# Kernel optimization log

Measured on AMD Instinct MI355X. Metric: run time of the kernel, lower is better.

## Reference

```python
import jax, jax.numpy as jnp
import numpy as np

D_MODEL = 1024
H = 16
D_K = D_MODEL // H


def setup_inputs() -> dict:
    key = jax.random.key(0)
    ks = jax.random.split(key, 12)
    B, S = 2, 2048
    scale = 1.0 / np.sqrt(D_MODEL)
    inp = {
        "q": jax.random.normal(ks[0], (B, S, D_MODEL), jnp.float32),
        "k": jax.random.normal(ks[1], (B, S, D_MODEL), jnp.float32),
        "v": jax.random.normal(ks[2], (B, S, D_MODEL), jnp.float32),
        "mask": jnp.ones((B, 1, S, S), jnp.int32),
        "w_q": jax.random.normal(ks[3], (D_MODEL, D_MODEL), jnp.float32) * scale,
        "b_q": jnp.zeros((D_MODEL,), jnp.float32),
        "w_k": jax.random.normal(ks[4], (D_MODEL, D_MODEL), jnp.float32) * scale,
        "b_k": jnp.zeros((D_MODEL,), jnp.float32),
        "w_v": jax.random.normal(ks[5], (D_MODEL, D_MODEL), jnp.float32) * scale,
        "b_v": jnp.zeros((D_MODEL,), jnp.float32),
        "w_o": jax.random.normal(ks[6], (D_MODEL, D_MODEL), jnp.float32) * scale,
        "b_o": jnp.zeros((D_MODEL,), jnp.float32),
    }
    return inp


def _split_heads(x):
    B, S, _ = x.shape
    return x.reshape(B, S, H, D_K).transpose(0, 2, 1, 3)  # [B,H,S,Dk]


def reference(q, k, v, mask, w_q, b_q, w_k, b_k, w_v, b_v, w_o, b_o):
    # Linear projections (torch Linear: x @ W^T + b)
    query = _split_heads(q @ w_q.T + b_q)
    key = _split_heads(k @ w_k.T + b_k)
    value = _split_heads(v @ w_v.T + b_v)

    # scaled dot-product attention: [B,H,S,S]
    scores = jnp.einsum("bhqd,bhkd->bhqk", query, key) / jnp.sqrt(
        jnp.asarray(D_K, query.dtype)
    )
    scores = jnp.where(mask == 0, jnp.asarray(-1e9, scores.dtype), scores)
    attn = jax.nn.softmax(scores, axis=-1)  # dropout p=0.0 -> identity
    out = jnp.einsum("bhqk,bhkd->bhqd", attn, value)  # [B,H,S,Dk]

    # combine heads -> [B,S,D_MODEL]
    B = out.shape[0]
    out = out.transpose(0, 2, 1, 3).reshape(B, -1, D_MODEL)
    return out @ w_o.T + b_o
```

## Files before the change

### kernel.cpp

```cpp
#include <hip/hip_runtime.h>
#include <hip/hip_bf16.h>

#define S_LEN 2048
#define BATCH 2
#define NH    16
#define DK    64
#define DM    1024

typedef __bf16 bf16x8 __attribute__((ext_vector_type(8)));
typedef float  f32x4  __attribute__((ext_vector_type(4)));
typedef ushort u16x8  __attribute__((ext_vector_type(8)));

__device__ __forceinline__ float bf2f(ushort u) {
    union { unsigned int i; float f; } v; v.i = ((unsigned int)u) << 16; return v.f;
}
__device__ __forceinline__ ushort f2bf(float f) {
    union { float f; unsigned int i; } v; v.f = f;
    unsigned int u = v.i;
    unsigned int r = u + 0x7fff + ((u >> 16) & 1);
    return (ushort)(r >> 16);
}
__device__ __forceinline__ ushort f2bf_fast(float f) {
    union { float f; unsigned int i; } v; v.f = f;
    return (ushort)((v.i + 0x8000u) >> 16);
}

__global__ void detect(const ushort* __restrict__ q, int* __restrict__ flags) {
    __shared__ int red[256];
    int tid = threadIdx.x;
    int cnt = 0;
    for (int i = tid; i < 2048; i += 256) {
        ushort e = q[2 * i];
        int ex = (e >> 7) & 0xFF;
        if (ex == 0 || (ex >= 107 && ex <= 147)) cnt++;
    }
    red[tid] = cnt;
    __syncthreads();
    for (int s = 128; s > 0; s >>= 1) {
        if (tid < s) red[tid] += red[tid + s];
        __syncthreads();
    }
    if (tid == 0) {
        flags[0] = (red[0] < 1229) ? 1 : 0;
        flags[1] = 0;
    }
}

__global__ void mask_check(const int* __restrict__ mask, int* __restrict__ flags) {
    const int total = BATCH * S_LEN * S_LEN / 4;
    int idx = blockIdx.x * blockDim.x + threadIdx.x;
    int stride = gridDim.x * blockDim.x;
    bool bad = false;
    for (int i = idx; i < total; i += stride) {
        int4 v = ((const int4*)mask)[i];
        if (v.x == 0 || v.y == 0 || v.z == 0 || v.w == 0) bad = true;
    }
    if (__any(bad)) {
        if ((threadIdx.x & 63) == 0) atomicOr(&flags[1], 1);
    }
}

#define NJOBS 11
struct CvtJobs { const void* src[NJOBS]; };

__device__ __constant__ const int g_cum[NJOBS + 1] = {
    0, 4194304, 8388608, 12582912, 13631488, 14680064, 15728640,
    16777216, 16778240, 16779264, 16780288, 16781312
};

__global__ __launch_bounds__(256) void convert_all(CvtJobs J, ushort* __restrict__ conv,
                                                   const int* __restrict__ flags) {
    bool isf32 = flags[0] != 0;
    const int total_chunks = 16781312 / 8;
    int c = blockIdx.x * blockDim.x + threadIdx.x;
    int stride = gridDim.x * blockDim.x;
    for (; c < total_chunks; c += stride) {
        int e = c * 8;
        int j = 0;
        while (j + 1 < NJOBS + 1 && e >= g_cum[j + 1]) j++;
        int local = e - g_cum[j];
        if (isf32) {
            const float* s = (const float*)J.src[j] + local;
            f32x4 a = *(const f32x4*)s;
            f32x4 b = *(const f32x4*)(s + 4);
            ushort o[8] = { f2bf(a[0]), f2bf(a[1]), f2bf(a[2]), f2bf(a[3]),
                            f2bf(b[0]), f2bf(b[1]), f2bf(b[2]), f2bf(b[3]) };
            *(ushort4*)&conv[e]     = *(ushort4*)&o[0];
            *(ushort4*)&conv[e + 4] = *(ushort4*)&o[4];
        } else {
            const ushort* s = (const ushort*)J.src[j] + local;
            bf16x8 v = *(const bf16x8*)s;
            *(bf16x8*)&conv[e] = v;
        }
    }
}

struct GArg { const ushort* x; const ushort* w; const ushort* bias; void* y; int split; };

#define ASTR 40

__global__ __launch_bounds__(256) void gemm_bt(GArg a0, GArg a1, GArg a2,
                                               const int* __restrict__ flags) {
    GArg A = (blockIdx.z == 0) ? a0 : (blockIdx.z == 1 ? a1 : a2);
    const int K = 1024, N = 1024;
    __shared__ ushort As[128 * ASTR];
    __shared__ ushort Bs[128 * ASTR];

    int tid = threadIdx.x;
    int w = tid >> 6, lane = tid & 63;
    int wm = (w >> 1) * 64, wn = (w & 1) * 64;
    int m0 = blockIdx.y * 128, n0 = blockIdx.x * 128;

    f32x4 acc[4][4] = {};

    int row0 = tid >> 2;
    int pos  = (tid & 3) * 8;
    int row1 = row0 + 64;

    int fr = lane & 15;
    int qd = lane >> 4;

    const ushort* xp = A.x;
    const ushort* wp = A.w;

    for (int k0 = 0; k0 < K; k0 += 32) {
        bf16x8 ax0 = *(const bf16x8*)&xp[(size_t)(m0 + row0) * K + k0 + pos];
        bf16x8 ax1 = *(const bf16x8*)&xp[(size_t)(m0 + row1) * K + k0 + pos];
        bf16x8 bx0 = *(const bf16x8*)&wp[(size_t)(n0 + row0) * K + k0 + pos];
        bf16x8 bx1 = *(const bf16x8*)&wp[(size_t)(n0 + row1) * K + k0 + pos];
        __syncthreads();
        *(bf16x8*)&As[row0 * ASTR + pos] = ax0;
        *(bf16x8*)&As[row1 * ASTR + pos] = ax1;
        *(bf16x8*)&Bs[row0 * ASTR + pos] = bx0;
        *(bf16x8*)&Bs[row1 * ASTR + pos] = bx1;
        __syncthreads();

        bf16x8 af[4], bfr[4];
#pragma unroll
        for (int i = 0; i < 4; i++) {
            af[i]  = *(const bf16x8*)&As[(wm + i * 16 + fr) * ASTR + qd * 8];
            bfr[i] = *(const bf16x8*)&Bs[(wn + i * 16 + fr) * ASTR + qd * 8];
        }
#pragma unroll
        for (int i = 0; i < 4; i++)
#pragma unroll
            for (int j = 0; j < 4; j++)
                acc[i][j] = __builtin_amdgcn_mfma_f32_16x16x32_bf16(af[i], bfr[j], acc[i][j], 0, 0, 0);
    }

    bool isf32 = flags[0] != 0;
    int crow = qd * 4;
    int ccol = fr;
#pragma unroll
    for (int j = 0; j < 4; j++) {
        int n_g = n0 + wn + j * 16 + ccol;
        float bias = bf2f(A.bias[n_g]);
#pragma unroll
        for (int i = 0; i < 4; i++) {
#pragma unroll
            for (int r = 0; r < 4; r++) {
                int m_g = m0 + wm + i * 16 + crow + r;
                float val = acc[i][j][r] + bias;
                if (A.split) {
                    int bb = m_g >> 11, s = m_g & 2047;
                    int h = n_g >> 6, d = n_g & 63;
                    ((ushort*)A.y)[((size_t)(bb * NH + h) * S_LEN + s) * DK + d] = f2bf(val);
                } else if (isf32) {
                    ((float*)A.y)[(size_t)m_g * N + n_g] = val;
                } else {
                    ((ushort*)A.y)[(size_t)m_g * N + n_g] = f2bf(val);
                }
            }
        }
    }
}

#define KSTR 80
#define VSTR 72
#define PSTR 76

__global__ __launch_bounds__(256) void attn(const ushort* __restrict__ qp,
                                            const ushort* __restrict__ kp,
                                            const ushort* __restrict__ vp,
                                            const int* __restrict__ mask,
                                            const int* __restrict__ flags,
                                            ushort* __restrict__ ctx) {
    __shared__ ushort Ks[64 * KSTR];
    __shared__ ushort Vt[64 * VSTR];
    __shared__ ushort Pb[4][16 * PSTR];

    int tid = threadIdx.x, w = tid >> 6, lane = tid & 63;
    int bh = blockIdx.y;
    int b = bh >> 4, h = bh & 15;
    int q0 = blockIdx.x * 64;

    const ushort* qb = qp + (size_t)bh * S_LEN * DK;
    const ushort* kb = kp + (size_t)bh * S_LEN * DK;
    const ushort* vb = vp + (size_t)bh * S_LEN * DK;
    const int* mb = mask + (size_t)b * S_LEN * S_LEN;
    bool do_mask = flags[1] != 0;

    int fr = lane & 15;
    int qd = lane >> 4;

    bf16x8 qf[2];
#pragma unroll
    for (int kc = 0; kc < 2; kc++)
        qf[kc] = *(const bf16x8*)&qb[(size_t)(q0 + w * 16 + fr) * DK + kc * 32 + qd * 8];

    f32x4 oacc[4] = {};
    float lrow[4] = {0.f, 0.f, 0.f, 0.f};

    int krow0 = tid >> 3;
    int kpos  = (tid & 7) * 8;
    int krow1 = krow0 + 32;
    int vc0 = w * 8, vc1 = (w + 4) * 8;

    const float cs = 0.125f * 1.44269504f;

    for (int k0 = 0; k0 < S_LEN; k0 += 64) {
        bf16x8 kx0 = *(const bf16x8*)&kb[(size_t)(k0 + krow0) * DK + kpos];
        bf16x8 kx1 = *(const bf16x8*)&kb[(size_t)(k0 + krow1) * DK + kpos];
        u16x8  vx0 = *(const u16x8*)&vb[(size_t)(k0 + lane) * DK + vc0];
        u16x8  vx1 = *(const u16x8*)&vb[(size_t)(k0 + lane) * DK + vc1];
        __syncthreads();
        *(bf16x8*)&Ks[krow0 * KSTR + kpos] = kx0;
        *(bf16x8*)&Ks[krow1 * KSTR + kpos] = kx1;
#pragma unroll
        for (int j = 0; j < 8; j++) {
            Vt[(vc0 + j) * VSTR + lane] = vx0[j];
            Vt[(vc1 + j) * VSTR + lane] = vx1[j];
        }
        __syncthreads();

        f32x4 sc[4] = {};
#pragma unroll
        for (int kc = 0; kc < 2; kc++) {
            bf16x8 kf[4];
#pragma unroll
            for (int ct = 0; ct < 4; ct++)
                kf[ct] = *(const bf16x8*)&Ks[(ct * 16 + fr) * KSTR + kc * 32 + qd * 8];
#pragma unroll
            for (int ct = 0; ct < 4; ct++)
                sc[ct] = __builtin_amdgcn_mfma_f32_16x16x32_bf16(qf[kc], kf[ct], sc[ct], 0, 0, 0);
        }

        if (do_mask) {
#pragma unroll
            for (int ct = 0; ct < 4; ct++)
#pragma unroll
                for (int r = 0; r < 4; r++) {
                    int qr = q0 + w * 16 + qd * 4 + r;
                    int kcid = k0 + ct * 16 + fr;
                    if (mb[(size_t)qr * S_LEN + kcid] == 0) sc[ct][r] = -1e9f;
                }
        }

#pragma unroll
        for (int ct = 0; ct < 4; ct++)
#pragma unroll
            for (int r = 0; r < 4; r++) {
                float p = __builtin_amdgcn_exp2f(fminf(sc[ct][r] * cs, 30.f));
                lrow[r] += p;
                Pb[w][(qd * 4 + r) * PSTR + ct * 16 + fr] = f2bf_fast(p);
            }

#pragma unroll
        for (int kk = 0; kk < 2; kk++) {
            bf16x8 pf = *(const bf16x8*)&Pb[w][fr * PSTR + kk * 32 + qd * 8];
            bf16x8 vf[4];
#pragma unroll
            for (int dt = 0; dt < 4; dt++)
                vf[dt] = *(const bf16x8*)&Vt[(dt * 16 + fr) * VSTR + kk * 32 + qd * 8];
#pragma unroll
            for (int dt = 0; dt < 4; dt++)
                oacc[dt] = __builtin_amdgcn_mfma_f32_16x16x32_bf16(pf, vf[dt], oacc[dt], 0, 0, 0);
        }
    }

#pragma unroll
    for (int r = 0; r < 4; r++) {
        float l = lrow[r];
        l += __shfl_xor(l, 1);
        l += __shfl_xor(l, 2);
        l += __shfl_xor(l, 4);
        l += __shfl_xor(l, 8);
        float inv = 1.0f / l;
        int qr = q0 + w * 16 + qd * 4 + r;
        size_t rowbase = ((size_t)(b * S_LEN + qr) * NH + h) * DK;
#pragma unroll
        for (int dt = 0; dt < 4; dt++)
            ctx[rowbase + dt * 16 + fr] = f2bf(oacc[dt][r] * inv);
    }
}

extern "C" void kernel_launch(void* const* d_in, const int* in_sizes, int n_in,
                              void* d_out, int out_size, void* d_ws, size_t ws_size,
                              hipStream_t stream) {
    const int* mask = (const int*)d_in[3];

    char* ws = (char*)d_ws;
    int*    flags = (int*)ws;
    ushort* conv  = (ushort*)(ws + 4096);
    const size_t conv_bytes = 16781312ull * 2;
    char* p = ws + 4096 + ((conv_bytes + 4095) & ~4095ull);
    size_t sz = (size_t)BATCH * NH * S_LEN * DK * sizeof(ushort);
    ushort* qp  = (ushort*)(p);
    ushort* kp  = (ushort*)(p + sz);
    ushort* vp  = (ushort*)(p + 2 * sz);
    ushort* ctx = (ushort*)(p + 3 * sz);

    ushort* qc  = conv + 0;
    ushort* kc  = conv + 4194304;
    ushort* vc  = conv + 8388608;
    ushort* wqc = conv + 12582912;
    ushort* wkc = conv + 13631488;
    ushort* wvc = conv + 14680064;
    ushort* woc = conv + 15728640;
    ushort* bqc = conv + 16777216;
    ushort* bkc = conv + 16778240;
    ushort* bvc = conv + 16779264;
    ushort* boc = conv + 16780288;

    detect<<<1, 256, 0, stream>>>((const ushort*)d_in[0], flags);
    mask_check<<<1024, 256, 0, stream>>>(mask, flags);

    CvtJobs J;
    J.src[0] = d_in[0];  J.src[1] = d_in[1];  J.src[2] = d_in[2];
    J.src[3] = d_in[4];  J.src[4] = d_in[6];  J.src[5] = d_in[8];
    J.src[6] = d_in[10]; J.src[7] = d_in[5];  J.src[8] = d_in[7];
    J.src[9] = d_in[9];  J.src[10] = d_in[11];
    convert_all<<<2048, 256, 0, stream>>>(J, conv, flags);

    GArg aq{qc, wqc, bqc, qp, 1};
    GArg ak{kc, wkc, bkc, kp, 1};
    GArg av{vc, wvc, bvc, vp, 1};
    gemm_bt<<<dim3(8, 32, 3), 256, 0, stream>>>(aq, ak, av, flags);

    attn<<<dim3(32, 32), 256, 0, stream>>>(qp, kp, vp, mask, flags, ctx);

    GArg ao{ctx, woc, boc, d_out, 0};
    gemm_bt<<<dim3(8, 32, 1), 256, 0, stream>>>(ao, ao, ao, flags);
}
```

Measured before the change: 308.9 us.

## Use async global-to-LDS loads with XOR swizzle, fold softmax scale into Q projection

Replaces the register-staged global-to-shared copies in the projection GEMM and the attention K tile with global_load_lds direct copies, using XOR-swizzled unpadded layouts to avoid bank conflicts. Folds the 1/sqrt(dk)*log2e scale into the Q projection epilogue. In attention, it computes the softmax row sums with an extra MFMA against a ones vector, which removes the shuffle reductions. It also converts P to bf16 by truncation and drops the clamp before exp2. Truncation and the missing clamp could affect accuracy or overflow, and bf16 row sums lose precision.

```diff
diff --git a/kernel.cpp b/kernel.cpp
--- a/kernel.cpp
+++ b/kernel.cpp
@@ -20,9 +20,11 @@
     unsigned int r = u + 0x7fff + ((u >> 16) & 1);
     return (ushort)(r >> 16);
 }
-__device__ __forceinline__ ushort f2bf_fast(float f) {
-    union { float f; unsigned int i; } v; v.f = f;
-    return (ushort)((v.i + 0x8000u) >> 16);
+
+__device__ __forceinline__ void async_copy16(const ushort* g, ushort* l) {
+    __builtin_amdgcn_global_load_lds(
+        (__attribute__((address_space(1))) void*)(g),
+        (__attribute__((address_space(3))) void*)(l), 16, 0, 0);
 }
 
 __global__ void detect(const ushort* __restrict__ q, int* __restrict__ flags) {
@@ -95,16 +97,14 @@
     }
 }
 
-struct GArg { const ushort* x; const ushort* w; const ushort* bias; void* y; int split; };
-
-#define ASTR 40
+struct GArg { const ushort* x; const ushort* w; const ushort* bias; void* y; int split; float scale; };
 
 __global__ __launch_bounds__(256) void gemm_bt(GArg a0, GArg a1, GArg a2,
                                                const int* __restrict__ flags) {
     GArg A = (blockIdx.z == 0) ? a0 : (blockIdx.z == 1 ? a1 : a2);
     const int K = 1024, N = 1024;
-    __shared__ ushort As[128 * ASTR];
-    __shared__ ushort Bs[128 * ASTR];
+    __shared__ ushort As[128 * 32];
+    __shared__ ushort Bs[128 * 32];
 
     int tid = threadIdx.x;
     int w = tid >> 6, lane = tid & 63;
@@ -113,33 +113,30 @@
 
     f32x4 acc[4][4] = {};
 
-    int row0 = tid >> 2;
-    int pos  = (tid & 3) * 8;
-    int row1 = row0 + 64;
+    int srow0 = w * 16 + (lane >> 2);
+    int srow1 = (w + 4) * 16 + (lane >> 2);
+    int schunk = ((lane & 3) ^ ((lane >> 3) & 3)) * 8;
 
     int fr = lane & 15;
     int qd = lane >> 4;
+    int fcp = (qd ^ ((fr >> 1) & 3)) * 8;
 
     const ushort* xp = A.x;
     const ushort* wp = A.w;
 
     for (int k0 = 0; k0 < K; k0 += 32) {
-        bf16x8 ax0 = *(const bf16x8*)&xp[(size_t)(m0 + row0) * K + k0 + pos];
-        bf16x8 ax1 = *(const bf16x8*)&xp[(size_t)(m0 + row1) * K + k0 + pos];
-        bf16x8 bx0 = *(const bf16x8*)&wp[(size_t)(n0 + row0) * K + k0 + pos];
-        bf16x8 bx1 = *(const bf16x8*)&wp[(size_t)(n0 + row1) * K + k0 + pos];
-        __syncthreads();
-        *(bf16x8*)&As[row0 * ASTR + pos] = ax0;
-        *(bf16x8*)&As[row1 * ASTR + pos] = ax1;
-        *(bf16x8*)&Bs[row0 * ASTR + pos] = bx0;
-        *(bf16x8*)&Bs[row1 * ASTR + pos] = bx1;
+        __syncthreads();
+        async_copy16(xp + (size_t)(m0 + srow0) * K + k0 + schunk, &As[w * 512]);
+        async_copy16(xp + (size_t)(m0 + srow1) * K + k0 + schunk, &As[(w + 4) * 512]);
+        async_copy16(wp + (size_t)(n0 + srow0) * K + k0 + schunk, &Bs[w * 512]);
+        async_copy16(wp + (size_t)(n0 + srow1) * K + k0 + schunk, &Bs[(w + 4) * 512]);
         __syncthreads();
 
         bf16x8 af[4], bfr[4];
 #pragma unroll
         for (int i = 0; i < 4; i++) {
-            af[i]  = *(const bf16x8*)&As[(wm + i * 16 + fr) * ASTR + qd * 8];
-            bfr[i] = *(const bf16x8*)&Bs[(wn + i * 16 + fr) * ASTR + qd * 8];
+            af[i]  = *(const bf16x8*)&As[(wm + i * 16 + fr) * 32 + fcp];
+            bfr[i] = *(const bf16x8*)&Bs[(wn + i * 16 + fr) * 32 + fcp];
         }
 #pragma unroll
         for (int i = 0; i < 4; i++)
@@ -160,7 +157,7 @@
 #pragma unroll
             for (int r = 0; r < 4; r++) {
                 int m_g = m0 + wm + i * 16 + crow + r;
-                float val = acc[i][j][r] + bias;
+                float val = (acc[i][j][r] + bias) * A.scale;
                 if (A.split) {
                     int bb = m_g >> 11, s = m_g & 2047;
                     int h = n_g >> 6, d = n_g & 63;
@@ -175,7 +172,6 @@
     }
 }
 
-#define KSTR 80
 #define VSTR 72
 #define PSTR 76
 
@@ -185,7 +181,7 @@
                                             const int* __restrict__ mask,
                                             const int* __restrict__ flags,
                                             ushort* __restrict__ ctx) {
-    __shared__ ushort Ks[64 * KSTR];
+    __shared__ ushort Ks[64 * 64];
     __shared__ ushort Vt[64 * VSTR];
     __shared__ ushort Pb[4][16 * PSTR];
 
@@ -208,24 +204,24 @@
     for (int kc = 0; kc < 2; kc++)
         qf[kc] = *(const bf16x8*)&qb[(size_t)(q0 + w * 16 + fr) * DK + kc * 32 + qd * 8];
 
+    bf16x8 ones;
+#pragma unroll
+    for (int j = 0; j < 8; j++) ones[j] = (__bf16)1.0f;
+
     f32x4 oacc[4] = {};
-    float lrow[4] = {0.f, 0.f, 0.f, 0.f};
-
-    int krow0 = tid >> 3;
-    int kpos  = (tid & 7) * 8;
-    int krow1 = krow0 + 32;
+    f32x4 lacc = {};
+
+    int kschunk = ((lane & 7) ^ ((lane >> 3) & 7)) * 8;
+    int ksrow0 = w * 8 + (lane >> 3);
+    int ksrow1 = (w + 4) * 8 + (lane >> 3);
     int vc0 = w * 8, vc1 = (w + 4) * 8;
 
-    const float cs = 0.125f * 1.44269504f;
-
     for (int k0 = 0; k0 < S_LEN; k0 += 64) {
-        bf16x8 kx0 = *(const bf16x8*)&kb[(size_t)(k0 + krow0) * DK + kpos];
-        bf16x8 kx1 = *(const bf16x8*)&kb[(size_t)(k0 + krow1) * DK + kpos];
-        u16x8  vx0 = *(const u16x8*)&vb[(size_t)(k0 + lane) * DK + vc0];
-        u16x8  vx1 = *(const u16x8*)&vb[(size_t)(k0 + lane) * DK + vc1];
-        __syncthreads();
-        *(bf16x8*)&Ks[krow0 * KSTR + kpos] = kx0;
-        *(bf16x8*)&Ks[krow1 * KSTR + kpos] = kx1;
+        u16x8 vx0 = *(const u16x8*)&vb[(size_t)(k0 + lane) * DK + vc0];
+        u16x8 vx1 = *(const u16x8*)&vb[(size_t)(k0 + lane) * DK + vc1];
+        __syncthreads();
+        async_copy16(&kb[(size_t)(k0 + ksrow0) * DK + kschunk], &Ks[w * 512]);
+        async_copy16(&kb[(size_t)(k0 + ksrow1) * DK + kschunk], &Ks[(w + 4) * 512]);
 #pragma unroll
         for (int j = 0; j < 8; j++) {
             Vt[(vc0 + j) * VSTR + lane] = vx0[j];
@@ -238,8 +234,10 @@
         for (int kc = 0; kc < 2; kc++) {
             bf16x8 kf[4];
 #pragma unroll
-            for (int ct = 0; ct < 4; ct++)
-                kf[ct] = *(const bf16x8*)&Ks[(ct * 16 + fr) * KSTR + kc * 32 + qd * 8];
+            for (int ct = 0; ct < 4; ct++) {
+                int key = ct * 16 + fr;
+                kf[ct] = *(const bf16x8*)&Ks[key * 64 + (((kc * 4 + qd) ^ (fr & 7)) * 8)];
+            }
 #pragma unroll
             for (int ct = 0; ct < 4; ct++)
                 sc[ct] = __builtin_amdgcn_mfma_f32_16x16x32_bf16(qf[kc], kf[ct], sc[ct], 0, 0, 0);
@@ -260,9 +258,9 @@
         for (int ct = 0; ct < 4; ct++)
 #pragma unroll
             for (int r = 0; r < 4; r++) {
-                float p = __builtin_amdgcn_exp2f(fminf(sc[ct][r] * cs, 30.f));
-                lrow[r] += p;
-                Pb[w][(qd * 4 + r) * PSTR + ct * 16 + fr] = f2bf_fast(p);
+                union { float f; ushort2 h; } t;
+                t.f = __builtin_amdgcn_exp2f(sc[ct][r]);
+                Pb[w][(qd * 4 + r) * PSTR + ct * 16 + fr] = t.h.y;
             }
 
 #pragma unroll
@@ -272,6 +270,7 @@
 #pragma unroll
             for (int dt = 0; dt < 4; dt++)
                 vf[dt] = *(const bf16x8*)&Vt[(dt * 16 + fr) * VSTR + kk * 32 + qd * 8];
+            lacc = __builtin_amdgcn_mfma_f32_16x16x32_bf16(pf, ones, lacc, 0, 0, 0);
 #pragma unroll
             for (int dt = 0; dt < 4; dt++)
                 oacc[dt] = __builtin_amdgcn_mfma_f32_16x16x32_bf16(pf, vf[dt], oacc[dt], 0, 0, 0);
@@ -280,12 +279,7 @@
 
 #pragma unroll
     for (int r = 0; r < 4; r++) {
-        float l = lrow[r];
-        l += __shfl_xor(l, 1);
-        l += __shfl_xor(l, 2);
-        l += __shfl_xor(l, 4);
-        l += __shfl_xor(l, 8);
-        float inv = 1.0f / l;
+        float inv = 1.0f / lacc[r];
         int qr = q0 + w * 16 + qd * 4 + r;
         size_t rowbase = ((size_t)(b * S_LEN + qr) * NH + h) * DK;
 #pragma unroll
@@ -332,13 +326,14 @@
     J.src[9] = d_in[9];  J.src[10] = d_in[11];
     convert_all<<<2048, 256, 0, stream>>>(J, conv, flags);
 
-    GArg aq{qc, wqc, bqc, qp, 1};
-    GArg ak{kc, wkc, bkc, kp, 1};
-    GArg av{vc, wvc, bvc, vp, 1};
+    const float cs = 0.125f * 1.44269504f;
+    GArg aq{qc, wqc, bqc, qp, 1, cs};
+    GArg ak{kc, wkc, bkc, kp, 1, 1.0f};
+    GArg av{vc, wvc, bvc, vp, 1, 1.0f};
     gemm_bt<<<dim3(8, 32, 3), 256, 0, stream>>>(aq, ak, av, flags);
 
     attn<<<dim3(32, 32), 256, 0, stream>>>(qp, kp, vp, mask, flags, ctx);
 
-    GArg ao{ctx, woc, boc, d_out, 0};
+    GArg ao{ctx, woc, boc, d_out, 0, 1.0f};
     gemm_bt<<<dim3(8, 32, 1), 256, 0, stream>>>(ao, ao, ao, flags);
 }
```

New measurement: 307.9 us. About the same (-0.3%).
